# Performance work log

Measured on AMD Instinct MI355X. Metric: run time of the kernel, lower is better.

Reference implementation:

```python
import jax, jax.numpy as jnp
import numpy as np

N = 50000          # nodes
E_RAND = 800000    # random edges (self-loops appended -> total 850000)
F_IN = 256         # features_num
H = 128            # hidden
HEADS = 4          # headslayers
C = 40             # num_class
OUTDIM = H + HEADS * H + H  # 768, cat of [x_lin, conv1, conv2]
LRELU = 0.01       # F.leaky_relu default slope
ATT_SLOPE = 0.2    # PyG GATConv negative_slope
BN_EPS = 1e-5


def setup_inputs() -> dict:
    key = jax.random.key(0)
    ks = jax.random.split(key, 20)
    src = jax.random.randint(ks[0], (E_RAND,), 0, N)
    dst = jax.random.randint(ks[1], (E_RAND,), 0, N)
    loops = jnp.arange(N, dtype=src.dtype)
    edge_index = jnp.stack([jnp.concatenate([src, loops]),
                            jnp.concatenate([dst, loops])], axis=0)
    g = lambda k, shape, fan: jax.random.normal(k, shape, jnp.float32) * (1.0 / np.sqrt(fan))
    return {
        "x": jax.random.normal(ks[2], (N, F_IN), jnp.float32),
        "edge_index": edge_index,
        # first_lin
        "fw_W": g(ks[3], (F_IN, H), F_IN), "fw_b": jnp.zeros((H,), jnp.float32),
        # conv1: GATConv(H, H, heads=HEADS)
        "c1_W": g(ks[4], (H, HEADS * H), H),
        "c1_as": g(ks[5], (HEADS, H), H), "c1_ad": g(ks[6], (HEADS, H), H),
        "c1_b": jnp.zeros((HEADS * H,), jnp.float32),
        # conv2: GATConv(HEADS*H, H, heads=1)
        "c2_W": g(ks[7], (HEADS * H, H), HEADS * H),
        "c2_as": g(ks[8], (1, H), H), "c2_ad": g(ks[9], (1, H), H),
        "c2_b": jnp.zeros((H,), jnp.float32),
        # batchnorms (training-mode batch stats)
        "bn1_g": jnp.ones((H,), jnp.float32), "bn1_b": jnp.zeros((H,), jnp.float32),
        "bn2_g": jnp.ones((HEADS * H,), jnp.float32), "bn2_b": jnp.zeros((HEADS * H,), jnp.float32),
        "bn3_g": jnp.ones((H,), jnp.float32), "bn3_b": jnp.zeros((H,), jnp.float32),
        # lin2
        "l2_W": g(ks[10], (OUTDIM, C), OUTDIM), "l2_b": jnp.zeros((C,), jnp.float32),
    }


def _batchnorm(x, gamma, beta):
    mu = jnp.mean(x, axis=0)
    var = jnp.mean(jnp.square(x - mu), axis=0)  # biased, as torch BN training
    return (x - mu) * (gamma / jnp.sqrt(var + BN_EPS)) + beta


def _gat_conv(x, edge_index, W, a_src, a_dst, bias, heads, out_dim):
    src, dst = edge_index[0], edge_index[1]
    h = (x @ W).reshape(-1, heads, out_dim)            # [N, heads, out]
    alpha_s = jnp.sum(h * a_src, axis=-1)              # [N, heads]
    alpha_d = jnp.sum(h * a_dst, axis=-1)              # [N, heads]
    e = alpha_s[src] + alpha_d[dst]                    # [E, heads]
    e = jnp.where(e >= 0, e, ATT_SLOPE * e)            # leaky_relu(0.2)
    # segment softmax over incoming edges of each dst node
    emax = jax.ops.segment_max(e, dst, num_segments=N)
    e = jnp.exp(e - emax[dst])
    denom = jax.ops.segment_sum(e, dst, num_segments=N)
    alpha = e / (denom[dst] + 1e-16)                   # [E, heads]
    msg = h[src] * alpha[:, :, None]                   # [E, heads, out]
    out = jax.ops.segment_sum(msg, dst, num_segments=N)
    return out.reshape(-1, heads * out_dim) + bias


def _lrelu(x):
    return jnp.where(x >= 0, x, LRELU * x)


def reference(x, edge_index, fw_W, fw_b, c1_W, c1_as, c1_ad, c1_b,
              c2_W, c2_as, c2_ad, c2_b, bn1_g, bn1_b, bn2_g, bn2_b,
              bn3_g, bn3_b, l2_W, l2_b):
    h = _lrelu(x @ fw_W + fw_b)
    h = _batchnorm(h, bn1_g, bn1_b)
    feats = [h]
    h = _lrelu(_gat_conv(h, edge_index, c1_W, c1_as, c1_ad, c1_b, HEADS, H))
    h = _batchnorm(h, bn2_g, bn2_b)
    feats.append(h)
    h = _lrelu(_gat_conv(h, edge_index, c2_W, c2_as, c2_ad, c2_b, 1, H))
    h = _batchnorm(h, bn3_g, bn3_b)
    feats.append(h)
    z = jnp.concatenate(feats, axis=1) @ l2_W + l2_b
    return jax.nn.log_softmax(z, axis=-1)
```

## Files before the change

### kernel.cpp

```cpp
#include <hip/hip_runtime.h>

#define INF_F __builtin_inff()

typedef unsigned short u16;
typedef __attribute__((ext_vector_type(8))) short s16x8;
typedef __attribute__((ext_vector_type(4))) float f32x4;

union U8 { uint4 q; s16x8 v; };

__device__ __forceinline__ float b2f(u16 u) {
    union { unsigned int i; float f; } v; v.i = ((unsigned int)u) << 16; return v.f;
}
__device__ __forceinline__ u16 f2b(float f) {
    union { float f; unsigned int i; } v; v.f = f;
    unsigned int r = (v.i + 0x7FFFu + ((v.i >> 16) & 1u)) >> 16;
    return (u16)r;
}
__device__ __forceinline__ void bf2x(unsigned int p, float& lo, float& hi) {
    union { unsigned int i; float f; } a, b;
    a.i = p << 16; b.i = p & 0xFFFF0000u;
    lo = a.f; hi = b.f;
}
__device__ __forceinline__ unsigned int packbf(float lo, float hi) {
    return (unsigned int)f2b(lo) | ((unsigned int)f2b(hi) << 16);
}

__device__ __forceinline__ void pack_one(const float* __restrict__ W, int K, int N,
                                         int Npad, u16* __restrict__ pb, int idx)
{
    int k = idx / Npad, n = idx - k * Npad;
    float v = (n < N) ? W[(size_t)k * N + n] : 0.f;
    int K5 = K >> 5;
    size_t o = ((size_t)(n >> 4) * K5 + (k >> 5)) * 512
             + ((size_t)((k >> 3) & 3)) * 128 + (n & 15) * 8 + (k & 7);
    pb[o] = f2b(v);
}

__launch_bounds__(256)
__global__ void k_prep(const float* __restrict__ fw_W, const float* __restrict__ c1_W,
                       const float* __restrict__ c2_W, const float* __restrict__ l2_W,
                       u16* __restrict__ pb_l1, u16* __restrict__ pb_c1,
                       u16* __restrict__ pb_c2, u16* __restrict__ pb_f,
                       const int* __restrict__ dst, int E, int* __restrict__ counts)
{
    int idx = blockIdx.x * 256 + threadIdx.x;
    if (idx < 32768) { pack_one(fw_W, 256, 128, 128, pb_l1, idx); return; }
    idx -= 32768;
    if (idx < 65536) { pack_one(c1_W, 128, 512, 512, pb_c1, idx); return; }
    idx -= 65536;
    if (idx < 65536) { pack_one(c2_W, 512, 128, 128, pb_c2, idx); return; }
    idx -= 65536;
    if (idx < 49152) { pack_one(l2_W, 768, 40, 64, pb_f, idx); return; }
    idx -= 49152;
    if (idx < E) atomicAdd(&counts[dst[idx]], 1);
}

template<int NFRAG, bool A_FP32, bool BN_A, bool BIAS, bool LRELU, int HEADS_PB>
__launch_bounds__(256)
__global__ void k_mgemm(const void* __restrict__ Av, int lda, int K,
                        const u16* __restrict__ pb,
                        u16* __restrict__ C, int ldc, int M,
                        const float* __restrict__ scale, const float* __restrict__ shift,
                        const float* __restrict__ bias,
                        const float* __restrict__ aw_s, const float* __restrict__ aw_d,
                        float* __restrict__ as_o, float* __restrict__ ad_o, int nheads)
{
    const int tid = threadIdx.x;
    const int w = tid >> 6, l = tid & 63;
    const int lo = l & 15, hi = l >> 4;
    const int row0 = blockIdx.y * 64 + w * 16;
    if (row0 >= M) return;
    const int cb0 = blockIdx.x * NFRAG;
    const int K5 = K >> 5;

    f32x4 acc[NFRAG];
    #pragma unroll
    for (int i = 0; i < NFRAG; ++i) acc[i] = (f32x4){0.f, 0.f, 0.f, 0.f};

    int arow = row0 + lo; if (arow >= M) arow = M - 1;

    for (int k5 = 0; k5 < K5; ++k5) {
        const int ak = k5 * 32 + hi * 8;
        float x[8];
        if (A_FP32) {
            const float* A = (const float*)Av + (size_t)arow * lda + ak;
            float4 v0 = *reinterpret_cast<const float4*>(A);
            float4 v1 = *reinterpret_cast<const float4*>(A + 4);
            x[0]=v0.x; x[1]=v0.y; x[2]=v0.z; x[3]=v0.w;
            x[4]=v1.x; x[5]=v1.y; x[6]=v1.z; x[7]=v1.w;
        } else {
            uint4 q = *reinterpret_cast<const uint4*>((const u16*)Av + (size_t)arow * lda + ak);
            bf2x(q.x, x[0], x[1]); bf2x(q.y, x[2], x[3]);
            bf2x(q.z, x[4], x[5]); bf2x(q.w, x[6], x[7]);
        }
        if (BN_A) {
            #pragma unroll
            for (int j = 0; j < 8; ++j) x[j] = fmaf(x[j], scale[ak + j], shift[ak + j]);
        }
        U8 au;
        au.q.x = packbf(x[0], x[1]); au.q.y = packbf(x[2], x[3]);
        au.q.z = packbf(x[4], x[5]); au.q.w = packbf(x[6], x[7]);
        s16x8 af = au.v;
        #pragma unroll
        for (int cb = 0; cb < NFRAG; ++cb) {
            s16x8 bf = *reinterpret_cast<const s16x8*>(
                pb + ((size_t)(cb0 + cb) * K5 + k5) * 512 + l * 8);
            acc[cb] = __builtin_amdgcn_mfma_f32_16x16x32_bf16(af, bf, acc[cb], 0, 0, 0);
        }
    }

    #pragma unroll
    for (int cb = 0; cb < NFRAG; ++cb) {
        int col = (cb0 + cb) * 16 + lo;
        #pragma unroll
        for (int p = 0; p < 4; ++p) {
            int r = row0 + hi * 4 + p;
            if (r < M) {
                float v = acc[cb][p];
                if (BIAS)  v += bias[col];
                if (LRELU) v = v >= 0.f ? v : 0.01f * v;
                C[(size_t)r * ldc + col] = f2b(v);
            }
        }
    }

    if (HEADS_PB > 0) {
        const int CBH = NFRAG / HEADS_PB;
        #pragma unroll
        for (int hl = 0; hl < HEADS_PB; ++hl) {
            float ps[4] = {0.f,0.f,0.f,0.f}, pd[4] = {0.f,0.f,0.f,0.f};
            #pragma unroll
            for (int cc = 0; cc < CBH; ++cc) {
                int cb = hl * CBH + cc;
                int col = (cb0 + cb) * 16 + lo;
                float ws = aw_s[col], wd = aw_d[col];
                #pragma unroll
                for (int p = 0; p < 4; ++p) {
                    ps[p] = fmaf(acc[cb][p], ws, ps[p]);
                    pd[p] = fmaf(acc[cb][p], wd, pd[p]);
                }
            }
            #pragma unroll
            for (int m = 1; m < 16; m <<= 1) {
                #pragma unroll
                for (int p = 0; p < 4; ++p) {
                    ps[p] += __shfl_xor(ps[p], m, 64);
                    pd[p] += __shfl_xor(pd[p], m, 64);
                }
            }
            if (lo == 0) {
                int h = (cb0 >> 3) + hl;
                #pragma unroll
                for (int p = 0; p < 4; ++p) {
                    int r = row0 + hi * 4 + p;
                    if (r < M) {
                        as_o[(size_t)r * nheads + h] = ps[p];
                        ad_o[(size_t)r * nheads + h] = pd[p];
                    }
                }
            }
        }
    }
}

__launch_bounds__(256)
__global__ void k_mfinal(const u16* __restrict__ h1, const u16* __restrict__ h2,
                         const u16* __restrict__ h3,
                         const float* __restrict__ scale, const float* __restrict__ shift,
                         const u16* __restrict__ pb, const float* __restrict__ bias,
                         float* __restrict__ out, int M)
{
    const int tid = threadIdx.x;
    const int w = tid >> 6, l = tid & 63;
    const int lo = l & 15, hi = l >> 4;
    const int row0 = blockIdx.x * 64 + w * 16;
    if (row0 >= M) return;
    const int K5 = 24;

    f32x4 acc[4];
    #pragma unroll
    for (int i = 0; i < 4; ++i) acc[i] = (f32x4){0.f, 0.f, 0.f, 0.f};

    int arow = row0 + lo; if (arow >= M) arow = M - 1;

    for (int k5 = 0; k5 < K5; ++k5) {
        const int kk = k5 * 32 + hi * 8;
        const u16* src; int ld, offk;
        if (kk < 128)      { src = h1; ld = 128; offk = kk; }
        else if (kk < 640) { src = h2; ld = 512; offk = kk - 128; }
        else               { src = h3; ld = 128; offk = kk - 640; }
        uint4 q = *reinterpret_cast<const uint4*>(src + (size_t)arow * ld + offk);
        float x[8];
        bf2x(q.x, x[0], x[1]); bf2x(q.y, x[2], x[3]);
        bf2x(q.z, x[4], x[5]); bf2x(q.w, x[6], x[7]);
        #pragma unroll
        for (int j = 0; j < 8; ++j) x[j] = fmaf(x[j], scale[kk + j], shift[kk + j]);
        U8 au;
        au.q.x = packbf(x[0], x[1]); au.q.y = packbf(x[2], x[3]);
        au.q.z = packbf(x[4], x[5]); au.q.w = packbf(x[6], x[7]);
        s16x8 af = au.v;
        #pragma unroll
        for (int cb = 0; cb < 4; ++cb) {
            s16x8 bf = *reinterpret_cast<const s16x8*>(pb + ((size_t)cb * K5 + k5) * 512 + l * 8);
            acc[cb] = __builtin_amdgcn_mfma_f32_16x16x32_bf16(af, bf, acc[cb], 0, 0, 0);
        }
    }

    #pragma unroll
    for (int p = 0; p < 4; ++p) {
        int r = row0 + hi * 4 + p;
        float z0 = acc[0][p] + bias[lo];
        float z1 = acc[1][p] + bias[16 + lo];
        float z2 = -INF_F;
        if (lo < 8) z2 = acc[2][p] + bias[32 + lo];
        float mx = fmaxf(fmaxf(z0, z1), z2);
        #pragma unroll
        for (int m = 1; m < 16; m <<= 1) mx = fmaxf(mx, __shfl_xor(mx, m, 64));
        float se = __expf(z0 - mx) + __expf(z1 - mx) + ((lo < 8) ? __expf(z2 - mx) : 0.f);
        #pragma unroll
        for (int m = 1; m < 16; m <<= 1) se += __shfl_xor(se, m, 64);
        float lse = mx + __logf(se);
        if (r < M) {
            out[(size_t)r * 40 + lo]      = z0 - lse;
            out[(size_t)r * 40 + 16 + lo] = z1 - lse;
            if (lo < 8) out[(size_t)r * 40 + 32 + lo] = z2 - lse;
        }
    }
}

__launch_bounds__(256)
__global__ void k_colstats(const u16* __restrict__ X, int M, int C,
                           float* __restrict__ psum, float* __restrict__ psq)
{
    const int CG  = C >> 3;
    const int RPI = 256 / CG;
    const int tid = threadIdx.x;
    const int cg  = tid & (CG - 1);
    const int ro  = tid / CG;
    const int nb  = gridDim.x;
    const int rows_chunk = (M + nb - 1) / nb;
    const int r0 = blockIdx.x * rows_chunk;
    const int r1 = min(M, r0 + rows_chunk);

    float s[8] = {}, q[8] = {};
    for (int r = r0 + ro; r < r1; r += RPI) {
        uint4 u = *reinterpret_cast<const uint4*>(X + (size_t)r * C + cg * 8);
        float x[8];
        bf2x(u.x, x[0], x[1]); bf2x(u.y, x[2], x[3]);
        bf2x(u.z, x[4], x[5]); bf2x(u.w, x[6], x[7]);
        #pragma unroll
        for (int j = 0; j < 8; ++j) { s[j] += x[j]; q[j] = fmaf(x[j], x[j], q[j]); }
    }

    __shared__ float lsum[8][256];
    __shared__ float lsq [8][256];
    #pragma unroll
    for (int j = 0; j < 8; ++j) { lsum[j][tid] = s[j]; lsq[j][tid] = q[j]; }
    __syncthreads();

    if (tid < CG) {
        #pragma unroll
        for (int j = 0; j < 8; ++j) {
            float ss = 0.f, qq = 0.f;
            for (int o = 0; o < RPI; ++o) {
                ss += lsum[j][o * CG + tid];
                qq += lsq [j][o * CG + tid];
            }
            psum[(size_t)blockIdx.x * C + tid * 8 + j] = ss;
            psq [(size_t)blockIdx.x * C + tid * 8 + j] = qq;
        }
    }
}

__launch_bounds__(256)
__global__ void k_colred(const float* __restrict__ psum, const float* __restrict__ psq,
                         const float* __restrict__ g, const float* __restrict__ b,
                         int nb, int M, int C,
                         float* __restrict__ scale, float* __restrict__ shift)
{
    int c = blockIdx.x * 4 + (threadIdx.x >> 6);
    int lane = threadIdx.x & 63;
    if (c >= C) return;
    float s = 0.f, q = 0.f;
    for (int l = lane; l < nb; l += 64) {
        s += psum[(size_t)l * C + c];
        q += psq [(size_t)l * C + c];
    }
    #pragma unroll
    for (int off = 32; off; off >>= 1) {
        s += __shfl_xor(s, off, 64);
        q += __shfl_xor(q, off, 64);
    }
    if (lane == 0) {
        float mu  = s / (float)M;
        float var = q / (float)M - mu * mu;
        float sc  = g[c] * rsqrtf(var + 1e-5f);
        scale[c] = sc;
        shift[c] = b[c] - mu * sc;
    }
}

__launch_bounds__(256)
__global__ void k_scan1(const int* __restrict__ counts, int n,
                        int* __restrict__ rowstart, int* __restrict__ tilesum)
{
    const int tid = threadIdx.x;
    const int lane = tid & 63, w = tid >> 6;
    const int i0 = blockIdx.x * 1024 + tid * 4;
    int v0 = 0, v1 = 0, v2 = 0, v3 = 0;
    if (i0 + 3 < n) {
        int4 q = *reinterpret_cast<const int4*>(counts + i0);
        v0 = q.x; v1 = q.y; v2 = q.z; v3 = q.w;
    } else if (i0 < n) {
        v0 = counts[i0];
        if (i0 + 1 < n) v1 = counts[i0 + 1];
        if (i0 + 2 < n) v2 = counts[i0 + 2];
    }
    int s1 = v0 + v1, s2 = s1 + v2, s3 = s2 + v3;
    int x = s3;
    #pragma unroll
    for (int off = 1; off < 64; off <<= 1) {
        int t = __shfl_up(x, off, 64);
        if (lane >= off) x += t;
    }
    __shared__ int wsum[4];
    if (lane == 63) wsum[w] = x;
    __syncthreads();
    int woff = 0;
    #pragma unroll
    for (int i = 0; i < 4; ++i)
        if (i < w) woff += wsum[i];
    int excl = woff + x - s3;
    if (i0 + 0 < n) rowstart[i0 + 1] = excl + v0;
    if (i0 + 1 < n) rowstart[i0 + 2] = excl + s1;
    if (i0 + 2 < n) rowstart[i0 + 3] = excl + s2;
    if (i0 + 3 < n) rowstart[i0 + 4] = excl + s3;
    if (tid == 255) tilesum[blockIdx.x] = wsum[0] + wsum[1] + wsum[2] + wsum[3];
}

__launch_bounds__(64)
__global__ void k_scan2(int* __restrict__ tilesum, int nt, int* __restrict__ rowstart)
{
    int lane = threadIdx.x;
    int carry = 0;
    for (int base = 0; base < nt; base += 64) {
        int v = (base + lane < nt) ? tilesum[base + lane] : 0;
        int x = v;
        #pragma unroll
        for (int off = 1; off < 64; off <<= 1) {
            int t = __shfl_up(x, off, 64);
            if (lane >= off) x += t;
        }
        if (base + lane < nt) tilesum[base + lane] = carry + x - v;
        carry += __shfl(x, 63, 64);
    }
    if (lane == 0) rowstart[0] = 0;
}

__launch_bounds__(256)
__global__ void k_scan3(int* __restrict__ rowstart, const int* __restrict__ tileoff, int n)
{
    int i = blockIdx.x * 256 + threadIdx.x;
    if (i < n) rowstart[i + 1] += tileoff[i >> 10];
}

__launch_bounds__(256)
__global__ void k_scatter(const int* __restrict__ ei, int E,
                          const int* __restrict__ rowstart,
                          int* __restrict__ fill, int* __restrict__ csr)
{
    int e = blockIdx.x * 256 + threadIdx.x;
    if (e >= E) return;
    int s = ei[e], d = ei[E + e];
    int pos = rowstart[d] + atomicAdd(&fill[d], 1);
    csr[pos] = s;
}

__launch_bounds__(256)
__global__ void k_gat_agg_h4(const u16* __restrict__ hp,
                             const float* __restrict__ as_, const float* __restrict__ ad_,
                             const int* __restrict__ rowstart, const int* __restrict__ csr,
                             const float* __restrict__ bias, u16* __restrict__ out, int Nn)
{
    int d = (int)((blockIdx.x * (size_t)blockDim.x + threadIdx.x) >> 6);
    int lane = threadIdx.x & 63;
    if (d >= Nn) return;
    const int h = lane >> 4;
    const int li = lane & 15;
    const int dim = li * 8;
    int e0 = rowstart[d], e1 = rowstart[d + 1];
    float adv = ad_[(size_t)d * 4 + h];

    float mx = -INF_F;
    for (int j = e0 + li; j < e1; j += 16) {
        int s = csr[j];
        float e = as_[(size_t)s * 4 + h] + adv;
        e = e >= 0.f ? e : 0.2f * e;
        mx = fmaxf(mx, e);
    }
    #pragma unroll
    for (int m = 1; m < 16; m <<= 1) mx = fmaxf(mx, __shfl_xor(mx, m, 64));

    float lsum = 0.f;
    float acc[8] = {};

    #define F4(J, A, U) { int jj = min((J), e1 - 1); int s_ = csr[jj];                \
        A = as_[(size_t)s_ * 4 + h];                                                  \
        U = *reinterpret_cast<const uint4*>(hp + ((size_t)s_ * 4 + h) * 128 + dim); }
    #define C4(A, U) { float e_ = A + adv; e_ = e_ >= 0.f ? e_ : 0.2f * e_;           \
        float w_ = __expf(e_ - mx); lsum += w_;                                       \
        float x_[8];                                                                  \
        bf2x(U.x, x_[0], x_[1]); bf2x(U.y, x_[2], x_[3]);                             \
        bf2x(U.z, x_[4], x_[5]); bf2x(U.w, x_[6], x_[7]);                             \
        _Pragma("unroll")                                                             \
        for (int t_ = 0; t_ < 8; ++t_) acc[t_] = fmaf(x_[t_], w_, acc[t_]); }

    float a0, a1, a2, a3, a4, a5, a6, a7;
    uint4 u0, u1, u2, u3, u4, u5, u6, u7;
    F4(e0 + 0, a0, u0); F4(e0 + 1, a1, u1); F4(e0 + 2, a2, u2); F4(e0 + 3, a3, u3);
    F4(e0 + 4, a4, u4); F4(e0 + 5, a5, u5); F4(e0 + 6, a6, u6); F4(e0 + 7, a7, u7);

    int j = e0;
    for (; j + 3 < e1; j += 4) {
        C4(a0, u0); C4(a1, u1); C4(a2, u2); C4(a3, u3);
        a0 = a4; u0 = u4; a1 = a5; u1 = u5; a2 = a6; u2 = u6; a3 = a7; u3 = u7;
        F4(j + 8, a4, u4); F4(j + 9, a5, u5); F4(j + 10, a6, u6); F4(j + 11, a7, u7);
    }
    if (j < e1)     C4(a0, u0);
    if (j + 1 < e1) C4(a1, u1);
    if (j + 2 < e1) C4(a2, u2);
    #undef F4
    #undef C4

    float inv = 1.f / (lsum + 1e-16f);
    const int ob = h * 128 + dim;
    float v[8];
    #pragma unroll
    for (int t = 0; t < 8; ++t) {
        float z = acc[t] * inv + bias[ob + t];
        v[t] = z >= 0.f ? z : 0.01f * z;
    }
    uint4 o;
    o.x = packbf(v[0], v[1]); o.y = packbf(v[2], v[3]);
    o.z = packbf(v[4], v[5]); o.w = packbf(v[6], v[7]);
    *reinterpret_cast<uint4*>(out + (size_t)d * 512 + ob) = o;
}

__launch_bounds__(256)
__global__ void k_gat_agg_h1(const u16* __restrict__ hp,
                             const float* __restrict__ as_, const float* __restrict__ ad_,
                             const int* __restrict__ rowstart, const int* __restrict__ csr,
                             const float* __restrict__ bias, u16* __restrict__ out, int Nn)
{
    int d = (int)((blockIdx.x * (size_t)blockDim.x + threadIdx.x) >> 6);
    int lane = threadIdx.x & 63;
    if (d >= Nn) return;
    const int dim = lane * 2;
    int e0 = rowstart[d], e1 = rowstart[d + 1];
    float adv = ad_[d];

    float mx = -INF_F;
    for (int j = e0 + lane; j < e1; j += 64) {
        int s = csr[j];
        float e = as_[s] + adv;
        e = e >= 0.f ? e : 0.2f * e;
        mx = fmaxf(mx, e);
    }
    #pragma unroll
    for (int m = 1; m < 64; m <<= 1) mx = fmaxf(mx, __shfl_xor(mx, m, 64));

    float lsum = 0.f, acc0 = 0.f, acc1 = 0.f;

    #define F1(J, A, U) { int jj = min((J), e1 - 1); int s_ = csr[jj];                \
        A = as_[s_];                                                                  \
        U = *reinterpret_cast<const unsigned int*>(hp + (size_t)s_ * 128 + dim); }
    #define C1(A, U) { float e_ = A + adv; e_ = e_ >= 0.f ? e_ : 0.2f * e_;           \
        float w_ = __expf(e_ - mx); float x0_, x1_; bf2x(U, x0_, x1_);                \
        lsum += w_; acc0 = fmaf(x0_, w_, acc0); acc1 = fmaf(x1_, w_, acc1); }

    float a0, a1, a2, a3, a4, a5, a6, a7;
    unsigned int u0, u1, u2, u3, u4, u5, u6, u7;
    F1(e0 + 0, a0, u0); F1(e0 + 1, a1, u1); F1(e0 + 2, a2, u2); F1(e0 + 3, a3, u3);
    F1(e0 + 4, a4, u4); F1(e0 + 5, a5, u5); F1(e0 + 6, a6, u6); F1(e0 + 7, a7, u7);

    int j = e0;
    for (; j + 3 < e1; j += 4) {
        C1(a0, u0); C1(a1, u1); C1(a2, u2); C1(a3, u3);
        a0 = a4; u0 = u4; a1 = a5; u1 = u5; a2 = a6; u2 = u6; a3 = a7; u3 = u7;
        F1(j + 8, a4, u4); F1(j + 9, a5, u5); F1(j + 10, a6, u6); F1(j + 11, a7, u7);
    }
    if (j < e1)     C1(a0, u0);
    if (j + 1 < e1) C1(a1, u1);
    if (j + 2 < e1) C1(a2, u2);
    #undef F1
    #undef C1

    float inv = 1.f / (lsum + 1e-16f);
    float v0 = acc0 * inv + bias[dim];
    float v1 = acc1 * inv + bias[dim + 1];
    v0 = v0 >= 0.f ? v0 : 0.01f * v0;
    v1 = v1 >= 0.f ? v1 : 0.01f * v1;
    *reinterpret_cast<unsigned int*>(out + (size_t)d * 128 + dim) = packbf(v0, v1);
}

extern "C" void kernel_launch(void* const* d_in, const int* in_sizes, int n_in,
                              void* d_out, int out_size, void* d_ws, size_t ws_size,
                              hipStream_t stream)
{
    const float* x     = (const float*)d_in[0];
    const int*   ei    = (const int*)  d_in[1];
    const float* fw_W  = (const float*)d_in[2];
    const float* fw_b  = (const float*)d_in[3];
    const float* c1_W  = (const float*)d_in[4];
    const float* c1_as = (const float*)d_in[5];
    const float* c1_ad = (const float*)d_in[6];
    const float* c1_b  = (const float*)d_in[7];
    const float* c2_W  = (const float*)d_in[8];
    const float* c2_as = (const float*)d_in[9];
    const float* c2_ad = (const float*)d_in[10];
    const float* c2_b  = (const float*)d_in[11];
    const float* bn1_g = (const float*)d_in[12];
    const float* bn1_b = (const float*)d_in[13];
    const float* bn2_g = (const float*)d_in[14];
    const float* bn2_b = (const float*)d_in[15];
    const float* bn3_g = (const float*)d_in[16];
    const float* bn3_b = (const float*)d_in[17];
    const float* l2_W  = (const float*)d_in[18];
    const float* l2_b  = (const float*)d_in[19];
    float* out = (float*)d_out;

    const int N = in_sizes[0] / 256;
    const int E = in_sizes[1] / 2;
    const int NB = 256;

    char* base = (char*)d_ws;
    size_t off = 0;
    auto alloc = [&](size_t bytes) -> void* {
        void* p = (void*)(base + off);
        off = (off + bytes + 255) & ~(size_t)255;
        return p;
    };
    int*   counts = (int*)  alloc((size_t)N * 4);
    int*   fill   = (int*)  alloc((size_t)N * 4);
    size_t zero_bytes = off;
    const int SCB = (N + 1023) / 1024;
    float* as1      = (float*)alloc((size_t)N * 4 * 4);
    float* ad1      = (float*)alloc((size_t)N * 4 * 4);
    float* as2      = (float*)alloc((size_t)N * 4);
    float* ad2      = (float*)alloc((size_t)N * 4);
    float* psum     = (float*)alloc((size_t)NB * 512 * 4);
    float* psq      = (float*)alloc((size_t)NB * 512 * 4);
    int*   rowstart = (int*)  alloc((size_t)(N + 1) * 4);
    int*   tilesum  = (int*)  alloc((size_t)SCB * 4);
    int*   csr      = (int*)  alloc((size_t)E * 4);
    float* scale768 = (float*)alloc(768 * 4);
    float* shift768 = (float*)alloc(768 * 4);
    u16*   pb_l1    = (u16*)  alloc((size_t)256 * 128 * 2);
    u16*   pb_c1    = (u16*)  alloc((size_t)128 * 512 * 2);
    u16*   pb_c2    = (u16*)  alloc((size_t)512 * 128 * 2);
    u16*   pb_f     = (u16*)  alloc((size_t)768 * 64 * 2);
    u16*   h1       = (u16*)  alloc((size_t)N * 128 * 2);
    u16*   h2       = (u16*)  alloc((size_t)N * 512 * 2);
    u16*   hp1      = (u16*)  alloc((size_t)N * 512 * 2);
    u16*   hp2      = hp1;
    u16*   h3       = hp1 + (size_t)N * 128;
    (void)ws_size; (void)n_in; (void)out_size;

    const int mb = (N + 63) / 64;
    const int wave_blocks = (int)(((size_t)N * 64 + 255) / 256);
    const int PK = 32768 + 65536 + 65536 + 49152;

    hipMemsetAsync(base, 0, zero_bytes, stream);

    k_prep<<<(PK + E + 255) / 256, 256, 0, stream>>>(
        fw_W, c1_W, c2_W, l2_W, pb_l1, pb_c1, pb_c2, pb_f, ei + E, E, counts);

    k_scan1<<<SCB, 256, 0, stream>>>(counts, N, rowstart, tilesum);
    k_scan2<<<1, 64, 0, stream>>>(tilesum, SCB, rowstart);
    k_scan3<<<(N + 255) / 256, 256, 0, stream>>>(rowstart, tilesum, N);

    k_scatter<<<(E + 255) / 256, 256, 0, stream>>>(ei, E, rowstart, fill, csr);

    k_mgemm<8, true, false, true, true, 0><<<dim3(1, mb), 256, 0, stream>>>(
        x, 256, 256, pb_l1, h1, 128, N, nullptr, nullptr, fw_b,
        nullptr, nullptr, nullptr, nullptr, 0);

    k_colstats<<<NB, 256, 0, stream>>>(h1, N, 128, psum, psq);
    k_colred<<<(128 + 3) / 4, 256, 0, stream>>>(psum, psq, bn1_g, bn1_b, NB, N, 128,
                                                scale768, shift768);

    k_mgemm<16, false, true, false, false, 2><<<dim3(2, mb), 256, 0, stream>>>(
        h1, 128, 128, pb_c1, hp1, 512, N, scale768, shift768, nullptr,
        c1_as, c1_ad, as1, ad1, 4);
    k_gat_agg_h4<<<wave_blocks, 256, 0, stream>>>(
        hp1, as1, ad1, rowstart, csr, c1_b, h2, N);

    k_colstats<<<NB, 256, 0, stream>>>(h2, N, 512, psum, psq);
    k_colred<<<(512 + 3) / 4, 256, 0, stream>>>(psum, psq, bn2_g, bn2_b, NB, N, 512,
                                                scale768 + 128, shift768 + 128);

    k_mgemm<8, false, true, false, false, 1><<<dim3(1, mb), 256, 0, stream>>>(
        h2, 512, 512, pb_c2, hp2, 128, N, scale768 + 128, shift768 + 128, nullptr,
        c2_as, c2_ad, as2, ad2, 1);
    k_gat_agg_h1<<<wave_blocks, 256, 0, stream>>>(
        hp2, as2, ad2, rowstart, csr, c2_b, h3, N);

    k_colstats<<<NB, 256, 0, stream>>>(h3, N, 128, psum, psq);
    k_colred<<<(128 + 3) / 4, 256, 0, stream>>>(psum, psq, bn3_g, bn3_b, NB, N, 128,
                                                scale768 + 640, shift768 + 640);

    k_mfinal<<<mb, 256, 0, stream>>>(h1, h2, h3, scale768, shift768, pb_f, l2_b, out, N);
}
```

Before: 511.5 us.

## Give each GEMM wave two row tiles and fold the scan2 kernel into scan3

Each wave in the MFMA GEMM and final-layer kernels now computes two 16-row tiles, so every B fragment load feeds two MFMAs and the grid halves. The conv1 GEMM is now launched as four column blocks, each holding one head. The single-block scan2 kernel is removed, and each scan3 block recomputes its tile prefix from tilesum with a wave reduction, which saves one launch. In exchange each wave uses more accumulator registers, and with fewer blocks on the GPU latency hiding may drop.

```diff
diff --git a/kernel.cpp b/kernel.cpp
--- a/kernel.cpp
+++ b/kernel.cpp
@@ -68,44 +68,56 @@
     const int tid = threadIdx.x;
     const int w = tid >> 6, l = tid & 63;
     const int lo = l & 15, hi = l >> 4;
-    const int row0 = blockIdx.y * 64 + w * 16;
+    const int row0 = blockIdx.y * 128 + w * 32;
     if (row0 >= M) return;
     const int cb0 = blockIdx.x * NFRAG;
     const int K5 = K >> 5;
 
-    f32x4 acc[NFRAG];
-    #pragma unroll
-    for (int i = 0; i < NFRAG; ++i) acc[i] = (f32x4){0.f, 0.f, 0.f, 0.f};
-
-    int arow = row0 + lo; if (arow >= M) arow = M - 1;
+    f32x4 acc[NFRAG][2];
+    #pragma unroll
+    for (int i = 0; i < NFRAG; ++i)
+        #pragma unroll
+        for (int s = 0; s < 2; ++s) acc[i][s] = (f32x4){0.f, 0.f, 0.f, 0.f};
+
+    int arow[2];
+    #pragma unroll
+    for (int s = 0; s < 2; ++s) {
+        int r = row0 + s * 16 + lo;
+        arow[s] = r < M ? r : M - 1;
+    }
 
     for (int k5 = 0; k5 < K5; ++k5) {
         const int ak = k5 * 32 + hi * 8;
-        float x[8];
-        if (A_FP32) {
-            const float* A = (const float*)Av + (size_t)arow * lda + ak;
-            float4 v0 = *reinterpret_cast<const float4*>(A);
-            float4 v1 = *reinterpret_cast<const float4*>(A + 4);
-            x[0]=v0.x; x[1]=v0.y; x[2]=v0.z; x[3]=v0.w;
-            x[4]=v1.x; x[5]=v1.y; x[6]=v1.z; x[7]=v1.w;
-        } else {
-            uint4 q = *reinterpret_cast<const uint4*>((const u16*)Av + (size_t)arow * lda + ak);
-            bf2x(q.x, x[0], x[1]); bf2x(q.y, x[2], x[3]);
-            bf2x(q.z, x[4], x[5]); bf2x(q.w, x[6], x[7]);
-        }
-        if (BN_A) {
-            #pragma unroll
-            for (int j = 0; j < 8; ++j) x[j] = fmaf(x[j], scale[ak + j], shift[ak + j]);
-        }
-        U8 au;
-        au.q.x = packbf(x[0], x[1]); au.q.y = packbf(x[2], x[3]);
-        au.q.z = packbf(x[4], x[5]); au.q.w = packbf(x[6], x[7]);
-        s16x8 af = au.v;
+        s16x8 af[2];
+        #pragma unroll
+        for (int s = 0; s < 2; ++s) {
+            float x[8];
+            if (A_FP32) {
+                const float* A = (const float*)Av + (size_t)arow[s] * lda + ak;
+                float4 v0 = *reinterpret_cast<const float4*>(A);
+                float4 v1 = *reinterpret_cast<const float4*>(A + 4);
+                x[0]=v0.x; x[1]=v0.y; x[2]=v0.z; x[3]=v0.w;
+                x[4]=v1.x; x[5]=v1.y; x[6]=v1.z; x[7]=v1.w;
+            } else {
+                uint4 q = *reinterpret_cast<const uint4*>((const u16*)Av + (size_t)arow[s] * lda + ak);
+                bf2x(q.x, x[0], x[1]); bf2x(q.y, x[2], x[3]);
+                bf2x(q.z, x[4], x[5]); bf2x(q.w, x[6], x[7]);
+            }
+            if (BN_A) {
+                #pragma unroll
+                for (int j = 0; j < 8; ++j) x[j] = fmaf(x[j], scale[ak + j], shift[ak + j]);
+            }
+            U8 au;
+            au.q.x = packbf(x[0], x[1]); au.q.y = packbf(x[2], x[3]);
+            au.q.z = packbf(x[4], x[5]); au.q.w = packbf(x[6], x[7]);
+            af[s] = au.v;
+        }
         #pragma unroll
         for (int cb = 0; cb < NFRAG; ++cb) {
             s16x8 bf = *reinterpret_cast<const s16x8*>(
                 pb + ((size_t)(cb0 + cb) * K5 + k5) * 512 + l * 8);
-            acc[cb] = __builtin_amdgcn_mfma_f32_16x16x32_bf16(af, bf, acc[cb], 0, 0, 0);
+            acc[cb][0] = __builtin_amdgcn_mfma_f32_16x16x32_bf16(af[0], bf, acc[cb][0], 0, 0, 0);
+            acc[cb][1] = __builtin_amdgcn_mfma_f32_16x16x32_bf16(af[1], bf, acc[cb][1], 0, 0, 0);
         }
     }
 
@@ -113,31 +125,33 @@
     for (int cb = 0; cb < NFRAG; ++cb) {
         int col = (cb0 + cb) * 16 + lo;
         #pragma unroll
-        for (int p = 0; p < 4; ++p) {
-            int r = row0 + hi * 4 + p;
-            if (r < M) {
-                float v = acc[cb][p];
-                if (BIAS)  v += bias[col];
-                if (LRELU) v = v >= 0.f ? v : 0.01f * v;
-                C[(size_t)r * ldc + col] = f2b(v);
+        for (int s = 0; s < 2; ++s) {
+            #pragma unroll
+            for (int p = 0; p < 4; ++p) {
+                int r = row0 + s * 16 + hi * 4 + p;
+                if (r < M) {
+                    float v = acc[cb][s][p];
+                    if (BIAS)  v += bias[col];
+                    if (LRELU) v = v >= 0.f ? v : 0.01f * v;
+                    C[(size_t)r * ldc + col] = f2b(v);
+                }
             }
         }
     }
 
     if (HEADS_PB > 0) {
-        const int CBH = NFRAG / HEADS_PB;
-        #pragma unroll
-        for (int hl = 0; hl < HEADS_PB; ++hl) {
+        const int h = (cb0 >> 3);
+        #pragma unroll
+        for (int s = 0; s < 2; ++s) {
             float ps[4] = {0.f,0.f,0.f,0.f}, pd[4] = {0.f,0.f,0.f,0.f};
             #pragma unroll
-            for (int cc = 0; cc < CBH; ++cc) {
-                int cb = hl * CBH + cc;
+            for (int cb = 0; cb < NFRAG; ++cb) {
                 int col = (cb0 + cb) * 16 + lo;
                 float ws = aw_s[col], wd = aw_d[col];
                 #pragma unroll
                 for (int p = 0; p < 4; ++p) {
-                    ps[p] = fmaf(acc[cb][p], ws, ps[p]);
-                    pd[p] = fmaf(acc[cb][p], wd, pd[p]);
+                    ps[p] = fmaf(acc[cb][s][p], ws, ps[p]);
+                    pd[p] = fmaf(acc[cb][s][p], wd, pd[p]);
                 }
             }
             #pragma unroll
@@ -149,10 +163,9 @@
                 }
             }
             if (lo == 0) {
-                int h = (cb0 >> 3) + hl;
                 #pragma unroll
                 for (int p = 0; p < 4; ++p) {
-                    int r = row0 + hi * 4 + p;
+                    int r = row0 + s * 16 + hi * 4 + p;
                     if (r < M) {
                         as_o[(size_t)r * nheads + h] = ps[p];
                         ad_o[(size_t)r * nheads + h] = pd[p];
@@ -173,15 +186,22 @@
     const int tid = threadIdx.x;
     const int w = tid >> 6, l = tid & 63;
     const int lo = l & 15, hi = l >> 4;
-    const int row0 = blockIdx.x * 64 + w * 16;
+    const int row0 = blockIdx.x * 128 + w * 32;
     if (row0 >= M) return;
     const int K5 = 24;
 
-    f32x4 acc[4];
-    #pragma unroll
-    for (int i = 0; i < 4; ++i) acc[i] = (f32x4){0.f, 0.f, 0.f, 0.f};
-
-    int arow = row0 + lo; if (arow >= M) arow = M - 1;
+    f32x4 acc[4][2];
+    #pragma unroll
+    for (int i = 0; i < 4; ++i)
+        #pragma unroll
+        for (int s = 0; s < 2; ++s) acc[i][s] = (f32x4){0.f, 0.f, 0.f, 0.f};
+
+    int arow[2];
+    #pragma unroll
+    for (int s = 0; s < 2; ++s) {
+        int r = row0 + s * 16 + lo;
+        arow[s] = r < M ? r : M - 1;
+    }
 
     for (int k5 = 0; k5 < K5; ++k5) {
         const int kk = k5 * 32 + hi * 8;
@@ -189,41 +209,49 @@
         if (kk < 128)      { src = h1; ld = 128; offk = kk; }
         else if (kk < 640) { src = h2; ld = 512; offk = kk - 128; }
         else               { src = h3; ld = 128; offk = kk - 640; }
-        uint4 q = *reinterpret_cast<const uint4*>(src + (size_t)arow * ld + offk);
-        float x[8];
-        bf2x(q.x, x[0], x[1]); bf2x(q.y, x[2], x[3]);
-        bf2x(q.z, x[4], x[5]); bf2x(q.w, x[6], x[7]);
-        #pragma unroll
-        for (int j = 0; j < 8; ++j) x[j] = fmaf(x[j], scale[kk + j], shift[kk + j]);
-        U8 au;
-        au.q.x = packbf(x[0], x[1]); au.q.y = packbf(x[2], x[3]);
-        au.q.z = packbf(x[4], x[5]); au.q.w = packbf(x[6], x[7]);
-        s16x8 af = au.v;
+        s16x8 af[2];
+        #pragma unroll
+        for (int s = 0; s < 2; ++s) {
+            uint4 q = *reinterpret_cast<const uint4*>(src + (size_t)arow[s] * ld + offk);
+            float x[8];
+            bf2x(q.x, x[0], x[1]); bf2x(q.y, x[2], x[3]);
+            bf2x(q.z, x[4], x[5]); bf2x(q.w, x[6], x[7]);
+            #pragma unroll
+            for (int j = 0; j < 8; ++j) x[j] = fmaf(x[j], scale[kk + j], shift[kk + j]);
+            U8 au;
+            au.q.x = packbf(x[0], x[1]); au.q.y = packbf(x[2], x[3]);
+            au.q.z = packbf(x[4], x[5]); au.q.w = packbf(x[6], x[7]);
+            af[s] = au.v;
+        }
         #pragma unroll
         for (int cb = 0; cb < 4; ++cb) {
             s16x8 bf = *reinterpret_cast<const s16x8*>(pb + ((size_t)cb * K5 + k5) * 512 + l * 8);
-            acc[cb] = __builtin_amdgcn_mfma_f32_16x16x32_bf16(af, bf, acc[cb], 0, 0, 0);
-        }
-    }
-
-    #pragma unroll
-    for (int p = 0; p < 4; ++p) {
-        int r = row0 + hi * 4 + p;
-        float z0 = acc[0][p] + bias[lo];
-        float z1 = acc[1][p] + bias[16 + lo];
-        float z2 = -INF_F;
-        if (lo < 8) z2 = acc[2][p] + bias[32 + lo];
-        float mx = fmaxf(fmaxf(z0, z1), z2);
-        #pragma unroll
-        for (int m = 1; m < 16; m <<= 1) mx = fmaxf(mx, __shfl_xor(mx, m, 64));
-        float se = __expf(z0 - mx) + __expf(z1 - mx) + ((lo < 8) ? __expf(z2 - mx) : 0.f);
-        #pragma unroll
-        for (int m = 1; m < 16; m <<= 1) se += __shfl_xor(se, m, 64);
-        float lse = mx + __logf(se);
-        if (r < M) {
-            out[(size_t)r * 40 + lo]      = z0 - lse;
-            out[(size_t)r * 40 + 16 + lo] = z1 - lse;
-            if (lo < 8) out[(size_t)r * 40 + 32 + lo] = z2 - lse;
+            acc[cb][0] = __builtin_amdgcn_mfma_f32_16x16x32_bf16(af[0], bf, acc[cb][0], 0, 0, 0);
+            acc[cb][1] = __builtin_amdgcn_mfma_f32_16x16x32_bf16(af[1], bf, acc[cb][1], 0, 0, 0);
+        }
+    }
+
+    #pragma unroll
+    for (int s = 0; s < 2; ++s) {
+        #pragma unroll
+        for (int p = 0; p < 4; ++p) {
+            int r = row0 + s * 16 + hi * 4 + p;
+            float z0 = acc[0][s][p] + bias[lo];
+            float z1 = acc[1][s][p] + bias[16 + lo];
+            float z2 = -INF_F;
+            if (lo < 8) z2 = acc[2][s][p] + bias[32 + lo];
+            float mx = fmaxf(fmaxf(z0, z1), z2);
+            #pragma unroll
+            for (int m = 1; m < 16; m <<= 1) mx = fmaxf(mx, __shfl_xor(mx, m, 64));
+            float se = __expf(z0 - mx) + __expf(z1 - mx) + ((lo < 8) ? __expf(z2 - mx) : 0.f);
+            #pragma unroll
+            for (int m = 1; m < 16; m <<= 1) se += __shfl_xor(se, m, 64);
+            float lse = mx + __logf(se);
+            if (r < M) {
+                out[(size_t)r * 40 + lo]      = z0 - lse;
+                out[(size_t)r * 40 + 16 + lo] = z1 - lse;
+                if (lo < 8) out[(size_t)r * 40 + 32 + lo] = z2 - lse;
+            }
         }
     }
 }
@@ -338,30 +366,22 @@
     if (tid == 255) tilesum[blockIdx.x] = wsum[0] + wsum[1] + wsum[2] + wsum[3];
 }
 
-__launch_bounds__(64)
-__global__ void k_scan2(int* __restrict__ tilesum, int nt, int* __restrict__ rowstart)
-{
-    int lane = threadIdx.x;
-    int carry = 0;
-    for (int base = 0; base < nt; base += 64) {
-        int v = (base + lane < nt) ? tilesum[base + lane] : 0;
-        int x = v;
-        #pragma unroll
-        for (int off = 1; off < 64; off <<= 1) {
-            int t = __shfl_up(x, off, 64);
-            if (lane >= off) x += t;
-        }
-        if (base + lane < nt) tilesum[base + lane] = carry + x - v;
-        carry += __shfl(x, 63, 64);
-    }
-    if (lane == 0) rowstart[0] = 0;
-}
-
-__launch_bounds__(256)
-__global__ void k_scan3(int* __restrict__ rowstart, const int* __restrict__ tileoff, int n)
-{
+__launch_bounds__(256)
+__global__ void k_scan3(int* __restrict__ rowstart, const int* __restrict__ tilesum, int n)
+{
+    const int tile = (int)((blockIdx.x * 256) >> 10);
+    __shared__ int s_off;
+    if (threadIdx.x < 64) {
+        int lane = threadIdx.x;
+        int v = (lane < tile) ? tilesum[lane] : 0;
+        #pragma unroll
+        for (int m = 1; m < 64; m <<= 1) v += __shfl_xor(v, m, 64);
+        if (lane == 0) s_off = v;
+    }
+    __syncthreads();
     int i = blockIdx.x * 256 + threadIdx.x;
-    if (i < n) rowstart[i + 1] += tileoff[i >> 10];
+    if (i < n) rowstart[i + 1] += s_off;
+    if (blockIdx.x == 0 && threadIdx.x == 0) rowstart[0] = 0;
 }
 
 __launch_bounds__(256)
@@ -566,7 +586,7 @@
     u16*   h3       = hp1 + (size_t)N * 128;
     (void)ws_size; (void)n_in; (void)out_size;
 
-    const int mb = (N + 63) / 64;
+    const int mb2 = (N + 127) / 128;
     const int wave_blocks = (int)(((size_t)N * 64 + 255) / 256);
     const int PK = 32768 + 65536 + 65536 + 49152;
 
@@ -576,12 +596,11 @@
         fw_W, c1_W, c2_W, l2_W, pb_l1, pb_c1, pb_c2, pb_f, ei + E, E, counts);
 
     k_scan1<<<SCB, 256, 0, stream>>>(counts, N, rowstart, tilesum);
-    k_scan2<<<1, 64, 0, stream>>>(tilesum, SCB, rowstart);
     k_scan3<<<(N + 255) / 256, 256, 0, stream>>>(rowstart, tilesum, N);
 
     k_scatter<<<(E + 255) / 256, 256, 0, stream>>>(ei, E, rowstart, fill, csr);
 
-    k_mgemm<8, true, false, true, true, 0><<<dim3(1, mb), 256, 0, stream>>>(
+    k_mgemm<8, true, false, true, true, 0><<<dim3(1, mb2), 256, 0, stream>>>(
         x, 256, 256, pb_l1, h1, 128, N, nullptr, nullptr, fw_b,
         nullptr, nullptr, nullptr, nullptr, 0);
 
@@ -589,7 +608,7 @@
     k_colred<<<(128 + 3) / 4, 256, 0, stream>>>(psum, psq, bn1_g, bn1_b, NB, N, 128,
                                                 scale768, shift768);
 
-    k_mgemm<16, false, true, false, false, 2><<<dim3(2, mb), 256, 0, stream>>>(
+    k_mgemm<8, false, true, false, false, 1><<<dim3(4, mb2), 256, 0, stream>>>(
         h1, 128, 128, pb_c1, hp1, 512, N, scale768, shift768, nullptr,
         c1_as, c1_ad, as1, ad1, 4);
     k_gat_agg_h4<<<wave_blocks, 256, 0, stream>>>(
@@ -599,7 +618,7 @@
     k_colred<<<(512 + 3) / 4, 256, 0, stream>>>(psum, psq, bn2_g, bn2_b, NB, N, 512,
                                                 scale768 + 128, shift768 + 128);
 
-    k_mgemm<8, false, true, false, false, 1><<<dim3(1, mb), 256, 0, stream>>>(
+    k_mgemm<8, false, true, false, false, 1><<<dim3(1, mb2), 256, 0, stream>>>(
         h2, 512, 512, pb_c2, hp2, 128, N, scale768 + 128, shift768 + 128, nullptr,
         c2_as, c2_ad, as2, ad2, 1);
     k_gat_agg_h1<<<wave_blocks, 256, 0, stream>>>(
@@ -609,5 +628,5 @@
     k_colred<<<(128 + 3) / 4, 256, 0, stream>>>(psum, psq, bn3_g, bn3_b, NB, N, 128,
                                                 scale768 + 640, shift768 + 640);
 
-    k_mfinal<<<mb, 256, 0, stream>>>(h1, h2, h3, scale768, shift768, pb_f, l2_b, out, N);
-}
+    k_mfinal<<<mb2, 256, 0, stream>>>(h1, h2, h3, scale768, shift768, pb_f, l2_b, out, N);
+}
```

Result: faster. 453.6 us (-11.3%).
